# Performance work log

Measured on AMD Instinct MI355X. Metric: run time of the kernel, lower is better.

The kernel has to match this reference:

```python
import jax, jax.numpy as jnp
import numpy as np

D = 256   # feature_dim
NQ = 512  # num query keypoints
NK = 512  # num key/value keypoints


def setup_inputs() -> dict:
    key = jax.random.key(0)
    ks = jax.random.split(key, 10)
    def w(k, shape, fan_in):
        return jax.random.normal(k, shape, dtype=jnp.float32) / np.sqrt(fan_in)
    inp = {
        "x": jax.random.normal(ks[0], (1, D, NQ), dtype=jnp.float32),
        "source": jax.random.normal(ks[1], (1, D, NK), dtype=jnp.float32),
        # MLPAttention score MLP: Conv1d(2D->D,k=1), ReLU, Conv1d(D->1,k=1)
        "w1": w(ks[2], (D, 2 * D), 2 * D),
        "b1": w(ks[3], (D,), 2 * D),
        "w2": w(ks[4], (1, D), D),
        "b2": w(ks[5], (1,), D),
        # outer MLP: Conv1d(2D->2D,k=1), ReLU, Conv1d(2D->D,k=1) with zero bias init
        "wa": w(ks[6], (2 * D, 2 * D), 2 * D),
        "ba": w(ks[7], (2 * D,), 2 * D),
        "wb": w(ks[8], (D, 2 * D), 2 * D),
        "bb": jnp.zeros((D,), dtype=jnp.float32),
    }
    return inp


def reference(x, source, w1, b1, w2, b2, wa, ba, wb, bb):
    d = x.shape[1]
    q = x[0]       # [D, nq]
    k = source[0]  # [D, nk]
    # cat((q broadcast over nk, k broadcast over nq)) then Conv1d(2D->D) is
    # equivalent to splitting w1 into query/key halves and broadcasting:
    w1q, w1k = w1[:, :d], w1[:, d:]
    aq = w1q @ q + b1[:, None]                       # [D, nq]
    ak = w1k @ k                                     # [D, nk]
    h = jax.nn.relu(aq[:, :, None] + ak[:, None, :])  # [D, nq, nk]
    scores = (jnp.einsum('d,dnm->nm', w2[0], h) + b2[0])[None]  # [1, nq, nk]
    prob = jax.nn.softmax(scores, axis=-1)
    message = jnp.einsum('bnm,bdm->bdn', prob, source)  # [1, D, nq]
    # outer MLP on cat([x, message], channel dim)
    cat = jnp.concatenate([x, message], axis=1)         # [1, 2D, nq]
    h2 = jax.nn.relu(jnp.einsum('oc,bcn->bon', wa, cat) + ba[None, :, None])
    y = jnp.einsum('oc,bcn->bon', wb, h2) + bb[None, :, None]  # [1, D, nq]
    return (y, scores)
```

## Files before the change

### kernel.cpp

```cpp
#include <hip/hip_runtime.h>
#include <hip/hip_bf16.h>

#define DD 256
#define NN 512

typedef __attribute__((ext_vector_type(8))) short short8;
typedef __attribute__((ext_vector_type(4))) float floatx4;

__device__ __forceinline__ unsigned short f2bf(float f) {
  unsigned u = __float_as_uint(f);
  u += 0x7FFFu + ((u >> 16) & 1u);
  return (unsigned short)(u >> 16);
}
__device__ __forceinline__ unsigned pack2(float a, float b) {
  return (unsigned)f2bf(a) | ((unsigned)f2bf(b) << 16);
}

__device__ __forceinline__ short8 ldfrag(const unsigned short* __restrict__ base,
                                         int row, int ld, int k, int lane) {
  return *(const short8*)(base + (row + (lane & 15)) * ld + k + ((lane >> 4) << 3));
}

__device__ __forceinline__ void gemm_acc(floatx4 acc[4],
    const unsigned short* __restrict__ A, int lda, int a_k0,
    const unsigned short* __restrict__ BT, int ldb, int b_k0,
    int K, int m0, int n0, int lane) {
  for (int k = 0; k < K; k += 32) {
    short8 a = ldfrag(A, m0, lda, a_k0 + k, lane);
#pragma unroll
    for (int nf = 0; nf < 4; ++nf) {
      short8 b = ldfrag(BT, n0 + nf * 16, ldb, b_k0 + k, lane);
      acc[nf] = __builtin_amdgcn_mfma_f32_16x16x32_bf16(a, b, acc[nf], 0, 0, 0);
    }
  }
}

__device__ __forceinline__ void acc_zero(floatx4 acc[4]) {
#pragma unroll
  for (int i = 0; i < 4; ++i) {
    acc[i][0] = 0.f; acc[i][1] = 0.f; acc[i][2] = 0.f; acc[i][3] = 0.f;
  }
}

__device__ __forceinline__ void ksplit_combine(floatx4 acc[4], float* red,
                                               int wave, int lane) {
  const int col = lane & 15;
  const int q = lane >> 4;
  if (wave > 0) {
    float* base = red + (wave - 1) * 1024;
#pragma unroll
    for (int nf = 0; nf < 4; ++nf)
#pragma unroll
      for (int r = 0; r < 4; ++r)
        base[(q * 4 + r) * 64 + nf * 16 + col] = acc[nf][r];
  }
  __syncthreads();
  if (wave == 0) {
#pragma unroll
    for (int nf = 0; nf < 4; ++nf)
#pragma unroll
      for (int r = 0; r < 4; ++r) {
        const int idx = (q * 4 + r) * 64 + nf * 16 + col;
        acc[nf][r] += red[idx] + red[1024 + idx] + red[2048 + idx];
      }
  }
}

template <bool COLBIAS, bool ROWBIAS, bool RELU, bool OUTBF>
__device__ __forceinline__ void gemm_epi(floatx4 acc[4],
    const float* __restrict__ bias, void* __restrict__ C, int ldc,
    int m0, int n0, int lane) {
  const int col = lane & 15;
  const int q = lane >> 4;
#pragma unroll
  for (int nf = 0; nf < 4; ++nf) {
    const int n = n0 + nf * 16 + col;
    const float cb = COLBIAS ? bias[n] : 0.0f;
#pragma unroll
    for (int r = 0; r < 4; ++r) {
      const int m = m0 + q * 4 + r;
      float v = acc[nf][r] + cb + (ROWBIAS ? bias[m] : 0.0f);
      if (RELU) v = fmaxf(v, 0.0f);
      if (OUTBF) ((unsigned short*)C)[m * ldc + n] = f2bf(v);
      else       ((float*)C)[m * ldc + n] = v;
    }
  }
}

__global__ __launch_bounds__(256) void prep_kernel(
    const float* __restrict__ x, const float* __restrict__ src,
    const float* __restrict__ w1, const float* __restrict__ wa,
    const float* __restrict__ wb,
    unsigned short* __restrict__ w1b, unsigned short* __restrict__ wab,
    unsigned short* __restrict__ wbb, unsigned short* __restrict__ srcb,
    unsigned short* __restrict__ xT, unsigned short* __restrict__ srcT) {
  const int bid = blockIdx.x;
  const int tid = threadIdx.x;
  if (bid < 640) {
    const float* in; unsigned short* out; int off;
    if (bid < 128)      { in = w1;  out = w1b; off = bid; }
    else if (bid < 384) { in = wa;  out = wab; off = bid - 128; }
    else if (bid < 512) { in = wb;  out = wbb; off = bid - 384; }
    else                { in = src; out = srcb; off = bid - 512; }
    const int i = off * 1024 + tid * 4;
    const float4 v = *(const float4*)(in + i);
    *(uint2*)(out + i) = make_uint2(pack2(v.x, v.y), pack2(v.z, v.w));
  } else {
    __shared__ float tile[32][33];
    const int b = bid - 640;
    const float* in = (b >> 7) ? src : x;
    unsigned short* out = (b >> 7) ? srcT : xT;
    const int t = b & 127;
    const int n0 = (t >> 3) * 32;
    const int d0 = (t & 7) * 32;
    const int tx = tid & 31, ty = tid >> 5;
#pragma unroll
    for (int i = ty; i < 32; i += 8)
      tile[i][tx] = in[(d0 + i) * NN + n0 + tx];
    __syncthreads();
#pragma unroll
    for (int i = ty; i < 32; i += 8)
      out[(n0 + i) * DD + d0 + tx] = f2bf(tile[tx][i]);
  }
}

__global__ __launch_bounds__(256) void aqak_kernel(
    const unsigned short* __restrict__ xT, const unsigned short* __restrict__ srcT,
    const unsigned short* __restrict__ w1b, const float* __restrict__ b1,
    float* __restrict__ aq, float* __restrict__ ak) {
  __shared__ float red[3072];
  const int tid = threadIdx.x;
  const int lane = tid & 63;
  const int wave = tid >> 6;
  const int m0 = blockIdx.y * 16;
  const int n0 = blockIdx.x * 64;
  const int z = blockIdx.z;
  const unsigned short* BT = z ? srcT : xT;

  floatx4 acc[4]; acc_zero(acc);
  gemm_acc(acc, w1b, NN, z * 256 + wave * 64, BT, DD, wave * 64, 64, m0, n0, lane);
  ksplit_combine(acc, red, wave, lane);
  if (wave == 0) {
    if (z == 0) gemm_epi<false, true, false, false>(acc, b1, aq, NN, m0, n0, lane);
    else        gemm_epi<false, false, false, false>(acc, nullptr, ak, NN, m0, n0, lane);
  }
}

__global__ __launch_bounds__(256) void scores_kernel(
    const float* __restrict__ aq, const float* __restrict__ ak,
    const float* __restrict__ w2, const float* __restrict__ b2,
    float* __restrict__ sc) {
  __shared__ float aqs[128][32];
  __shared__ float aks[128][32];
  __shared__ float w2s[DD];

  const int tid = threadIdx.x;
  const int n0 = blockIdx.x * 32;
  const int m0 = blockIdx.y * 32;
  const int tn = tid & 31;
  const int tm4 = (tid >> 5) * 4;

  w2s[tid] = w2[tid];

  float s0 = 0.f, s1 = 0.f, s2 = 0.f, s3 = 0.f;

  for (int d0 = 0; d0 < DD; d0 += 128) {
    __syncthreads();
#pragma unroll
    for (int k = 0; k < 16; ++k) {
      const int idx = k * 256 + tid;
      const int r = idx >> 5, cc = idx & 31;
      aqs[r][cc] = aq[(d0 + r) * NN + n0 + cc];
      aks[r][cc] = ak[(d0 + r) * NN + m0 + cc];
    }
    __syncthreads();

    for (int dd = 0; dd < 128; ++dd) {
      const float w = w2s[d0 + dd];
      const float a = aqs[dd][tn];
      const float4 akv = *(const float4*)&aks[dd][tm4];
      s0 += w * fmaxf(a + akv.x, 0.f);
      s1 += w * fmaxf(a + akv.y, 0.f);
      s2 += w * fmaxf(a + akv.z, 0.f);
      s3 += w * fmaxf(a + akv.w, 0.f);
    }
  }

  const float bv = b2[0];
  float4 o;
  o.x = s0 + bv; o.y = s1 + bv; o.z = s2 + bv; o.w = s3 + bv;
  *(float4*)&sc[(n0 + tn) * NN + m0 + tm4] = o;
}

__global__ __launch_bounds__(256) void msgT_kernel(
    const float* __restrict__ sc, const unsigned short* __restrict__ srcb,
    unsigned short* __restrict__ msgTb) {
  __shared__ unsigned short Ap[16][520];
  __shared__ float red[3072];
  __shared__ float smax[16][16];
  __shared__ float ssum[16][16];
  __shared__ float rst[16][2];

  const int tid = threadIdx.x;
  const int lane = tid & 63;
  const int wave = tid >> 6;
  const int n0 = blockIdx.y * 16;
  const int d0 = blockIdx.x * 64;

  const int r = tid >> 4;
  const int seg = tid & 15;
  float4 v[8];
  const float* rp = sc + (n0 + r) * NN + seg * 32;
#pragma unroll
  for (int i = 0; i < 8; ++i) v[i] = *(const float4*)(rp + i * 4);

  float mx = -3.0e38f;
#pragma unroll
  for (int i = 0; i < 8; ++i)
    mx = fmaxf(mx, fmaxf(fmaxf(v[i].x, v[i].y), fmaxf(v[i].z, v[i].w)));
  smax[r][seg] = mx;
  __syncthreads();
  if (seg == 0) {
    float m2 = smax[r][0];
#pragma unroll
    for (int i = 1; i < 16; ++i) m2 = fmaxf(m2, smax[r][i]);
    rst[r][0] = m2;
  }
  __syncthreads();
  mx = rst[r][0];

  float sum = 0.f;
#pragma unroll
  for (int i = 0; i < 8; ++i) {
    v[i].x = __expf(v[i].x - mx); v[i].y = __expf(v[i].y - mx);
    v[i].z = __expf(v[i].z - mx); v[i].w = __expf(v[i].w - mx);
    sum += v[i].x + v[i].y + v[i].z + v[i].w;
  }
  ssum[r][seg] = sum;
  __syncthreads();
  if (seg == 0) {
    float s2 = ssum[r][0];
#pragma unroll
    for (int i = 1; i < 16; ++i) s2 += ssum[r][i];
    rst[r][1] = s2;
  }
  __syncthreads();
  const float inv = 1.0f / rst[r][1];
#pragma unroll
  for (int i = 0; i < 8; ++i) {
    *(unsigned*)&Ap[r][seg * 32 + i * 4]     = pack2(v[i].x * inv, v[i].y * inv);
    *(unsigned*)&Ap[r][seg * 32 + i * 4 + 2] = pack2(v[i].z * inv, v[i].w * inv);
  }
  __syncthreads();

  floatx4 acc[4]; acc_zero(acc);
  const int k0w = wave * 128;
  const int arow = lane & 15;
  const int koff = (lane >> 4) << 3;
  for (int k = 0; k < 128; k += 32) {
    short8 a = *(const short8*)&Ap[arow][k0w + k + koff];
#pragma unroll
    for (int nf = 0; nf < 4; ++nf) {
      short8 b = ldfrag(srcb, d0 + nf * 16, NN, k0w + k, lane);
      acc[nf] = __builtin_amdgcn_mfma_f32_16x16x32_bf16(a, b, acc[nf], 0, 0, 0);
    }
  }
  ksplit_combine(acc, red, wave, lane);
  if (wave == 0)
    gemm_epi<false, false, false, true>(acc, nullptr, msgTb, DD, n0, d0, lane);
}

__global__ __launch_bounds__(256) void h2T_kernel(
    const unsigned short* __restrict__ xT, const unsigned short* __restrict__ msgTb,
    const unsigned short* __restrict__ wab, const float* __restrict__ ba,
    unsigned short* __restrict__ h2Tb) {
  __shared__ float red[3072];
  const int tid = threadIdx.x;
  const int lane = tid & 63;
  const int wave = tid >> 6;
  const int m0 = blockIdx.y * 16;
  const int n0 = blockIdx.x * 64;

  floatx4 acc[4]; acc_zero(acc);
  const unsigned short* A = (wave < 2) ? xT : msgTb;
  gemm_acc(acc, A, DD, (wave & 1) * 128, wab, NN, wave * 128, 128, m0, n0, lane);
  ksplit_combine(acc, red, wave, lane);
  if (wave == 0)
    gemm_epi<true, false, true, true>(acc, ba, h2Tb, NN, m0, n0, lane);
}

__global__ __launch_bounds__(256) void y_kernel(
    const unsigned short* __restrict__ wbb, const unsigned short* __restrict__ h2Tb,
    const float* __restrict__ bb, float* __restrict__ y) {
  __shared__ float red[3072];
  const int tid = threadIdx.x;
  const int lane = tid & 63;
  const int wave = tid >> 6;
  const int m0 = blockIdx.y * 16;
  const int n0 = blockIdx.x * 64;

  floatx4 acc[4]; acc_zero(acc);
  gemm_acc(acc, wbb, NN, wave * 128, h2Tb, NN, wave * 128, 128, m0, n0, lane);
  ksplit_combine(acc, red, wave, lane);
  if (wave == 0)
    gemm_epi<false, true, false, false>(acc, bb, y, NN, m0, n0, lane);
}

extern "C" void kernel_launch(void* const* d_in, const int* in_sizes, int n_in,
                              void* d_out, int out_size, void* d_ws, size_t ws_size,
                              hipStream_t stream) {
  (void)in_sizes; (void)n_in; (void)out_size; (void)ws_size;

  const float* x   = (const float*)d_in[0];
  const float* src = (const float*)d_in[1];
  const float* w1  = (const float*)d_in[2];
  const float* b1  = (const float*)d_in[3];
  const float* w2  = (const float*)d_in[4];
  const float* b2  = (const float*)d_in[5];
  const float* wa  = (const float*)d_in[6];
  const float* ba  = (const float*)d_in[7];
  const float* wb  = (const float*)d_in[8];
  const float* bb  = (const float*)d_in[9];

  float* y_out  = (float*)d_out;
  float* sc_out = (float*)d_out + 131072;

  char* ws = (char*)d_ws;
  unsigned short* w1b   = (unsigned short*)(ws);
  unsigned short* wab   = (unsigned short*)(ws + (256 << 10));
  unsigned short* wbb   = (unsigned short*)(ws + (768 << 10));
  unsigned short* srcb  = (unsigned short*)(ws + (1024 << 10));
  unsigned short* xT    = (unsigned short*)(ws + (1280 << 10));
  unsigned short* srcT  = (unsigned short*)(ws + (1536 << 10));
  unsigned short* msgTb = (unsigned short*)(ws + (1792 << 10));
  unsigned short* h2Tb  = (unsigned short*)(ws + (2048 << 10));
  float*          aq    = (float*)(ws + (2560 << 10));
  float*          ak    = (float*)(ws + (3072 << 10));

  prep_kernel<<<896, 256, 0, stream>>>(x, src, w1, wa, wb,
                                       w1b, wab, wbb, srcb, xT, srcT);
  aqak_kernel<<<dim3(8, 16, 2), 256, 0, stream>>>(xT, srcT, w1b, b1, aq, ak);
  scores_kernel<<<dim3(16, 16), 256, 0, stream>>>(aq, ak, w2, b2, sc_out);
  msgT_kernel<<<dim3(4, 32), 256, 0, stream>>>(sc_out, srcb, msgTb);
  h2T_kernel<<<dim3(8, 32), 256, 0, stream>>>(xT, msgTb, wab, ba, h2Tb);
  y_kernel<<<dim3(8, 16), 256, 0, stream>>>(wbb, h2Tb, bb, y_out);
}
```

Baseline: 108.4 us.

## Halve GEMM tile widths and split scores over D with atomic accumulation

All MFMA GEMM kernels move from 64-wide to 32-wide output tiles, which doubles the block count to fill more compute units on the device. The scores kernel is split along the feature dimension into two blocks that atomically add into the scores buffer, which prep now pre-initializes with the b2 bias. The softmax load pattern in msgT is changed to strided float4 loads for coalescing. This trades more blocks, duplicated A-fragment loads and float atomics (non-deterministic summation order) for better occupancy of a small problem.

```diff
diff --git a/kernel.cpp b/kernel.cpp
--- a/kernel.cpp
+++ b/kernel.cpp
@@ -21,59 +21,63 @@
   return *(const short8*)(base + (row + (lane & 15)) * ld + k + ((lane >> 4) << 3));
 }
 
-__device__ __forceinline__ void gemm_acc(floatx4 acc[4],
+template <int NF>
+__device__ __forceinline__ void acc_zero(floatx4 acc[NF]) {
+#pragma unroll
+  for (int i = 0; i < NF; ++i) {
+    acc[i][0] = 0.f; acc[i][1] = 0.f; acc[i][2] = 0.f; acc[i][3] = 0.f;
+  }
+}
+
+template <int NF>
+__device__ __forceinline__ void gemm_acc(floatx4 acc[NF],
     const unsigned short* __restrict__ A, int lda, int a_k0,
     const unsigned short* __restrict__ BT, int ldb, int b_k0,
     int K, int m0, int n0, int lane) {
   for (int k = 0; k < K; k += 32) {
     short8 a = ldfrag(A, m0, lda, a_k0 + k, lane);
 #pragma unroll
-    for (int nf = 0; nf < 4; ++nf) {
+    for (int nf = 0; nf < NF; ++nf) {
       short8 b = ldfrag(BT, n0 + nf * 16, ldb, b_k0 + k, lane);
       acc[nf] = __builtin_amdgcn_mfma_f32_16x16x32_bf16(a, b, acc[nf], 0, 0, 0);
     }
   }
 }
 
-__device__ __forceinline__ void acc_zero(floatx4 acc[4]) {
-#pragma unroll
-  for (int i = 0; i < 4; ++i) {
-    acc[i][0] = 0.f; acc[i][1] = 0.f; acc[i][2] = 0.f; acc[i][3] = 0.f;
-  }
-}
-
-__device__ __forceinline__ void ksplit_combine(floatx4 acc[4], float* red,
+template <int NF>
+__device__ __forceinline__ void ksplit_combine(floatx4 acc[NF], float* red,
                                                int wave, int lane) {
+  const int W = 16 * NF;
   const int col = lane & 15;
   const int q = lane >> 4;
   if (wave > 0) {
-    float* base = red + (wave - 1) * 1024;
-#pragma unroll
-    for (int nf = 0; nf < 4; ++nf)
+    float* base = red + (wave - 1) * 16 * W;
+#pragma unroll
+    for (int nf = 0; nf < NF; ++nf)
 #pragma unroll
       for (int r = 0; r < 4; ++r)
-        base[(q * 4 + r) * 64 + nf * 16 + col] = acc[nf][r];
+        base[(q * 4 + r) * W + nf * 16 + col] = acc[nf][r];
   }
   __syncthreads();
   if (wave == 0) {
 #pragma unroll
-    for (int nf = 0; nf < 4; ++nf)
+    for (int nf = 0; nf < NF; ++nf)
 #pragma unroll
       for (int r = 0; r < 4; ++r) {
-        const int idx = (q * 4 + r) * 64 + nf * 16 + col;
-        acc[nf][r] += red[idx] + red[1024 + idx] + red[2048 + idx];
+        const int idx = (q * 4 + r) * W + nf * 16 + col;
+        acc[nf][r] += red[idx] + red[16 * W + idx] + red[32 * W + idx];
       }
   }
 }
 
-template <bool COLBIAS, bool ROWBIAS, bool RELU, bool OUTBF>
-__device__ __forceinline__ void gemm_epi(floatx4 acc[4],
+template <int NF, bool COLBIAS, bool ROWBIAS, bool RELU, bool OUTBF>
+__device__ __forceinline__ void gemm_epi(floatx4 acc[NF],
     const float* __restrict__ bias, void* __restrict__ C, int ldc,
     int m0, int n0, int lane) {
   const int col = lane & 15;
   const int q = lane >> 4;
 #pragma unroll
-  for (int nf = 0; nf < 4; ++nf) {
+  for (int nf = 0; nf < NF; ++nf) {
     const int n = n0 + nf * 16 + col;
     const float cb = COLBIAS ? bias[n] : 0.0f;
 #pragma unroll
@@ -90,10 +94,11 @@
 __global__ __launch_bounds__(256) void prep_kernel(
     const float* __restrict__ x, const float* __restrict__ src,
     const float* __restrict__ w1, const float* __restrict__ wa,
-    const float* __restrict__ wb,
+    const float* __restrict__ wb, const float* __restrict__ b2,
     unsigned short* __restrict__ w1b, unsigned short* __restrict__ wab,
     unsigned short* __restrict__ wbb, unsigned short* __restrict__ srcb,
-    unsigned short* __restrict__ xT, unsigned short* __restrict__ srcT) {
+    unsigned short* __restrict__ xT, unsigned short* __restrict__ srcT,
+    float* __restrict__ sc) {
   const int bid = blockIdx.x;
   const int tid = threadIdx.x;
   if (bid < 640) {
@@ -105,7 +110,7 @@
     const int i = off * 1024 + tid * 4;
     const float4 v = *(const float4*)(in + i);
     *(uint2*)(out + i) = make_uint2(pack2(v.x, v.y), pack2(v.z, v.w));
-  } else {
+  } else if (bid < 896) {
     __shared__ float tile[32][33];
     const int b = bid - 640;
     const float* in = (b >> 7) ? src : x;
@@ -121,6 +126,11 @@
 #pragma unroll
     for (int i = ty; i < 32; i += 8)
       out[(n0 + i) * DD + d0 + tx] = f2bf(tile[tx][i]);
+  } else {
+    const float bv = b2[0];
+    const int i = (bid - 896) * 1024 + tid * 4;
+    float4 o; o.x = bv; o.y = bv; o.z = bv; o.w = bv;
+    *(float4*)(sc + i) = o;
   }
 }
 
@@ -128,75 +138,71 @@
     const unsigned short* __restrict__ xT, const unsigned short* __restrict__ srcT,
     const unsigned short* __restrict__ w1b, const float* __restrict__ b1,
     float* __restrict__ aq, float* __restrict__ ak) {
-  __shared__ float red[3072];
+  __shared__ float red[1536];
   const int tid = threadIdx.x;
   const int lane = tid & 63;
   const int wave = tid >> 6;
   const int m0 = blockIdx.y * 16;
-  const int n0 = blockIdx.x * 64;
+  const int n0 = blockIdx.x * 32;
   const int z = blockIdx.z;
   const unsigned short* BT = z ? srcT : xT;
 
-  floatx4 acc[4]; acc_zero(acc);
-  gemm_acc(acc, w1b, NN, z * 256 + wave * 64, BT, DD, wave * 64, 64, m0, n0, lane);
-  ksplit_combine(acc, red, wave, lane);
+  floatx4 acc[2]; acc_zero<2>(acc);
+  gemm_acc<2>(acc, w1b, NN, z * 256 + wave * 64, BT, DD, wave * 64, 64, m0, n0, lane);
+  ksplit_combine<2>(acc, red, wave, lane);
   if (wave == 0) {
-    if (z == 0) gemm_epi<false, true, false, false>(acc, b1, aq, NN, m0, n0, lane);
-    else        gemm_epi<false, false, false, false>(acc, nullptr, ak, NN, m0, n0, lane);
+    if (z == 0) gemm_epi<2, false, true, false, false>(acc, b1, aq, NN, m0, n0, lane);
+    else        gemm_epi<2, false, false, false, false>(acc, nullptr, ak, NN, m0, n0, lane);
   }
 }
 
 __global__ __launch_bounds__(256) void scores_kernel(
     const float* __restrict__ aq, const float* __restrict__ ak,
-    const float* __restrict__ w2, const float* __restrict__ b2,
-    float* __restrict__ sc) {
+    const float* __restrict__ w2, float* __restrict__ sc) {
   __shared__ float aqs[128][32];
   __shared__ float aks[128][32];
-  __shared__ float w2s[DD];
+  __shared__ float w2s[128];
 
   const int tid = threadIdx.x;
   const int n0 = blockIdx.x * 32;
   const int m0 = blockIdx.y * 32;
+  const int d0 = blockIdx.z * 128;
   const int tn = tid & 31;
   const int tm4 = (tid >> 5) * 4;
 
-  w2s[tid] = w2[tid];
+  if (tid < 128) w2s[tid] = w2[d0 + tid];
+#pragma unroll
+  for (int k = 0; k < 16; ++k) {
+    const int idx = k * 256 + tid;
+    const int r = idx >> 5, cc = idx & 31;
+    aqs[r][cc] = aq[(d0 + r) * NN + n0 + cc];
+    aks[r][cc] = ak[(d0 + r) * NN + m0 + cc];
+  }
+  __syncthreads();
 
   float s0 = 0.f, s1 = 0.f, s2 = 0.f, s3 = 0.f;
-
-  for (int d0 = 0; d0 < DD; d0 += 128) {
-    __syncthreads();
-#pragma unroll
-    for (int k = 0; k < 16; ++k) {
-      const int idx = k * 256 + tid;
-      const int r = idx >> 5, cc = idx & 31;
-      aqs[r][cc] = aq[(d0 + r) * NN + n0 + cc];
-      aks[r][cc] = ak[(d0 + r) * NN + m0 + cc];
-    }
-    __syncthreads();
-
-    for (int dd = 0; dd < 128; ++dd) {
-      const float w = w2s[d0 + dd];
-      const float a = aqs[dd][tn];
-      const float4 akv = *(const float4*)&aks[dd][tm4];
-      s0 += w * fmaxf(a + akv.x, 0.f);
-      s1 += w * fmaxf(a + akv.y, 0.f);
-      s2 += w * fmaxf(a + akv.z, 0.f);
-      s3 += w * fmaxf(a + akv.w, 0.f);
-    }
-  }
-
-  const float bv = b2[0];
-  float4 o;
-  o.x = s0 + bv; o.y = s1 + bv; o.z = s2 + bv; o.w = s3 + bv;
-  *(float4*)&sc[(n0 + tn) * NN + m0 + tm4] = o;
+  for (int dd = 0; dd < 128; ++dd) {
+    const float w = w2s[dd];
+    const float a = aqs[dd][tn];
+    const float4 akv = *(const float4*)&aks[dd][tm4];
+    s0 += w * fmaxf(a + akv.x, 0.f);
+    s1 += w * fmaxf(a + akv.y, 0.f);
+    s2 += w * fmaxf(a + akv.z, 0.f);
+    s3 += w * fmaxf(a + akv.w, 0.f);
+  }
+
+  float* p = &sc[(n0 + tn) * NN + m0 + tm4];
+  atomicAdd(p + 0, s0);
+  atomicAdd(p + 1, s1);
+  atomicAdd(p + 2, s2);
+  atomicAdd(p + 3, s3);
 }
 
 __global__ __launch_bounds__(256) void msgT_kernel(
     const float* __restrict__ sc, const unsigned short* __restrict__ srcb,
     unsigned short* __restrict__ msgTb) {
   __shared__ unsigned short Ap[16][520];
-  __shared__ float red[3072];
+  __shared__ float red[1536];
   __shared__ float smax[16][16];
   __shared__ float ssum[16][16];
   __shared__ float rst[16][2];
@@ -205,22 +211,22 @@
   const int lane = tid & 63;
   const int wave = tid >> 6;
   const int n0 = blockIdx.y * 16;
-  const int d0 = blockIdx.x * 64;
+  const int d0 = blockIdx.x * 32;
 
   const int r = tid >> 4;
-  const int seg = tid & 15;
+  const int c = tid & 15;
   float4 v[8];
-  const float* rp = sc + (n0 + r) * NN + seg * 32;
-#pragma unroll
-  for (int i = 0; i < 8; ++i) v[i] = *(const float4*)(rp + i * 4);
+  const float* rp = sc + (n0 + r) * NN + c * 4;
+#pragma unroll
+  for (int i = 0; i < 8; ++i) v[i] = *(const float4*)(rp + i * 64);
 
   float mx = -3.0e38f;
 #pragma unroll
   for (int i = 0; i < 8; ++i)
     mx = fmaxf(mx, fmaxf(fmaxf(v[i].x, v[i].y), fmaxf(v[i].z, v[i].w)));
-  smax[r][seg] = mx;
-  __syncthreads();
-  if (seg == 0) {
+  smax[r][c] = mx;
+  __syncthreads();
+  if (c == 0) {
     float m2 = smax[r][0];
 #pragma unroll
     for (int i = 1; i < 16; ++i) m2 = fmaxf(m2, smax[r][i]);
@@ -236,9 +242,9 @@
     v[i].z = __expf(v[i].z - mx); v[i].w = __expf(v[i].w - mx);
     sum += v[i].x + v[i].y + v[i].z + v[i].w;
   }
-  ssum[r][seg] = sum;
-  __syncthreads();
-  if (seg == 0) {
+  ssum[r][c] = sum;
+  __syncthreads();
+  if (c == 0) {
     float s2 = ssum[r][0];
 #pragma unroll
     for (int i = 1; i < 16; ++i) s2 += ssum[r][i];
@@ -248,62 +254,62 @@
   const float inv = 1.0f / rst[r][1];
 #pragma unroll
   for (int i = 0; i < 8; ++i) {
-    *(unsigned*)&Ap[r][seg * 32 + i * 4]     = pack2(v[i].x * inv, v[i].y * inv);
-    *(unsigned*)&Ap[r][seg * 32 + i * 4 + 2] = pack2(v[i].z * inv, v[i].w * inv);
-  }
-  __syncthreads();
-
-  floatx4 acc[4]; acc_zero(acc);
+    *(unsigned*)&Ap[r][c * 4 + i * 64]     = pack2(v[i].x * inv, v[i].y * inv);
+    *(unsigned*)&Ap[r][c * 4 + i * 64 + 2] = pack2(v[i].z * inv, v[i].w * inv);
+  }
+  __syncthreads();
+
+  floatx4 acc[2]; acc_zero<2>(acc);
   const int k0w = wave * 128;
   const int arow = lane & 15;
   const int koff = (lane >> 4) << 3;
   for (int k = 0; k < 128; k += 32) {
     short8 a = *(const short8*)&Ap[arow][k0w + k + koff];
 #pragma unroll
-    for (int nf = 0; nf < 4; ++nf) {
+    for (int nf = 0; nf < 2; ++nf) {
       short8 b = ldfrag(srcb, d0 + nf * 16, NN, k0w + k, lane);
       acc[nf] = __builtin_amdgcn_mfma_f32_16x16x32_bf16(a, b, acc[nf], 0, 0, 0);
     }
   }
-  ksplit_combine(acc, red, wave, lane);
+  ksplit_combine<2>(acc, red, wave, lane);
   if (wave == 0)
-    gemm_epi<false, false, false, true>(acc, nullptr, msgTb, DD, n0, d0, lane);
+    gemm_epi<2, false, false, false, true>(acc, nullptr, msgTb, DD, n0, d0, lane);
 }
 
 __global__ __launch_bounds__(256) void h2T_kernel(
     const unsigned short* __restrict__ xT, const unsigned short* __restrict__ msgTb,
     const unsigned short* __restrict__ wab, const float* __restrict__ ba,
     unsigned short* __restrict__ h2Tb) {
-  __shared__ float red[3072];
+  __shared__ float red[1536];
   const int tid = threadIdx.x;
   const int lane = tid & 63;
   const int wave = tid >> 6;
   const int m0 = blockIdx.y * 16;
-  const int n0 = blockIdx.x * 64;
-
-  floatx4 acc[4]; acc_zero(acc);
+  const int n0 = blockIdx.x * 32;
+
+  floatx4 acc[2]; acc_zero<2>(acc);
   const unsigned short* A = (wave < 2) ? xT : msgTb;
-  gemm_acc(acc, A, DD, (wave & 1) * 128, wab, NN, wave * 128, 128, m0, n0, lane);
-  ksplit_combine(acc, red, wave, lane);
+  gemm_acc<2>(acc, A, DD, (wave & 1) * 128, wab, NN, wave * 128, 128, m0, n0, lane);
+  ksplit_combine<2>(acc, red, wave, lane);
   if (wave == 0)
-    gemm_epi<true, false, true, true>(acc, ba, h2Tb, NN, m0, n0, lane);
+    gemm_epi<2, true, false, true, true>(acc, ba, h2Tb, NN, m0, n0, lane);
 }
 
 __global__ __launch_bounds__(256) void y_kernel(
     const unsigned short* __restrict__ wbb, const unsigned short* __restrict__ h2Tb,
     const float* __restrict__ bb, float* __restrict__ y) {
-  __shared__ float red[3072];
+  __shared__ float red[1536];
   const int tid = threadIdx.x;
   const int lane = tid & 63;
   const int wave = tid >> 6;
   const int m0 = blockIdx.y * 16;
-  const int n0 = blockIdx.x * 64;
-
-  floatx4 acc[4]; acc_zero(acc);
-  gemm_acc(acc, wbb, NN, wave * 128, h2Tb, NN, wave * 128, 128, m0, n0, lane);
-  ksplit_combine(acc, red, wave, lane);
+  const int n0 = blockIdx.x * 32;
+
+  floatx4 acc[2]; acc_zero<2>(acc);
+  gemm_acc<2>(acc, wbb, NN, wave * 128, h2Tb, NN, wave * 128, 128, m0, n0, lane);
+  ksplit_combine<2>(acc, red, wave, lane);
   if (wave == 0)
-    gemm_epi<false, true, false, false>(acc, bb, y, NN, m0, n0, lane);
+    gemm_epi<2, false, true, false, false>(acc, bb, y, NN, m0, n0, lane);
 }
 
 extern "C" void kernel_launch(void* const* d_in, const int* in_sizes, int n_in,
@@ -337,11 +343,11 @@
   float*          aq    = (float*)(ws + (2560 << 10));
   float*          ak    = (float*)(ws + (3072 << 10));
 
-  prep_kernel<<<896, 256, 0, stream>>>(x, src, w1, wa, wb,
-                                       w1b, wab, wbb, srcb, xT, srcT);
-  aqak_kernel<<<dim3(8, 16, 2), 256, 0, stream>>>(xT, srcT, w1b, b1, aq, ak);
-  scores_kernel<<<dim3(16, 16), 256, 0, stream>>>(aq, ak, w2, b2, sc_out);
-  msgT_kernel<<<dim3(4, 32), 256, 0, stream>>>(sc_out, srcb, msgTb);
-  h2T_kernel<<<dim3(8, 32), 256, 0, stream>>>(xT, msgTb, wab, ba, h2Tb);
-  y_kernel<<<dim3(8, 16), 256, 0, stream>>>(wbb, h2Tb, bb, y_out);
-}
+  prep_kernel<<<1152, 256, 0, stream>>>(x, src, w1, wa, wb, b2,
+                                        w1b, wab, wbb, srcb, xT, srcT, sc_out);
+  aqak_kernel<<<dim3(16, 16, 2), 256, 0, stream>>>(xT, srcT, w1b, b1, aq, ak);
+  scores_kernel<<<dim3(16, 16, 2), 256, 0, stream>>>(aq, ak, w2, sc_out);
+  msgT_kernel<<<dim3(8, 32), 256, 0, stream>>>(sc_out, srcb, msgTb);
+  h2T_kernel<<<dim3(16, 32), 256, 0, stream>>>(xT, msgTb, wab, ba, h2Tb);
+  y_kernel<<<dim3(16, 16), 256, 0, stream>>>(wbb, h2Tb, bb, y_out);
+}
```

Result: slower. 112.7 us (+3.9%).
